# Performance work log

Measured on AMD Instinct MI355X. Metric: run time of the kernel, lower is better.

Reference implementation:

```python
import jax, jax.numpy as jnp
import numpy as np

LEAKY_ALPHA = 0.2  # tf.nn.leaky_relu default

B, N, F_IN, HID = 1, 8192, 512, 256


def setup_inputs() -> dict:
    key = jax.random.key(0)
    ks = jax.random.split(key, 4)
    seq = jax.random.normal(ks[0], (B, N, F_IN), dtype=jnp.float32)
    bias_mat = jnp.zeros((B, N, N), dtype=jnp.float32)  # 0 = edge present (fully connected mask)
    W = jax.random.normal(ks[1], (F_IN, HID), dtype=jnp.float32) * (1.0 / np.sqrt(F_IN))
    a1 = jax.random.normal(ks[2], (HID, 1), dtype=jnp.float32) * (1.0 / np.sqrt(HID))
    b1 = jnp.zeros((1,), dtype=jnp.float32)
    a2 = jax.random.normal(ks[3], (HID, 1), dtype=jnp.float32) * (1.0 / np.sqrt(HID))
    b2 = jnp.zeros((1,), dtype=jnp.float32)
    bias_zero = jnp.zeros((HID,), dtype=jnp.float32)
    return {"seq": seq, "bias_mat": bias_mat, "W": W, "a1": a1, "b1": b1,
            "a2": a2, "b2": b2, "bias_zero": bias_zero}


def reference(seq, bias_mat, W, a1, b1, a2, b2, bias_zero):
    # Conv1D(kernel=1, no bias) == per-node linear projection
    seq_fts = jnp.einsum('bnf,fh->bnh', seq, W)            # [B,N,H]
    f_1 = jnp.einsum('bnh,ho->bno', seq_fts, a1) + b1      # [B,N,1]
    f_2 = jnp.einsum('bnh,ho->bno', seq_fts, a2) + b2      # [B,N,1]
    logits = f_1 + jnp.swapaxes(f_2, 1, 2)                 # [B,N,N] outer-sum
    scores = jnp.where(logits > 0, logits, LEAKY_ALPHA * logits) + bias_mat
    coefs = jax.nn.softmax(scores, axis=-1)                # masked softmax over neighbors
    vals = jnp.einsum('bnm,bmh->bnh', coefs, seq_fts)      # aggregation
    ret = vals + bias_zero
    return jax.nn.elu(ret)
```

## Files before the change

### kernel.cpp

```cpp
#include <hip/hip_runtime.h>
#include <hip/hip_bf16.h>
#include <stdint.h>

#define NN 8192
#define FIN 512
#define HID 256

typedef short bf16x8 __attribute__((ext_vector_type(8)));
typedef float f32x4 __attribute__((ext_vector_type(4)));

__device__ __forceinline__ uint32_t pk2(float lo, float hi) {
  uint32_t a = __float_as_uint(lo), b = __float_as_uint(hi);
  a = (a + 0x7FFFu + ((a >> 16) & 1u)) >> 16;
  b = (b + 0x7FFFu + ((b >> 16) & 1u)) >> 16;
  return a | (b << 16);
}

#define OFF_SEQB   0u
#define OFF_WTB    8388608u
#define OFF_FTST   8650752u
#define OFF_F1     12845056u
#define OFF_F2     12877824u
#define OFF_Z      12910592u
#define OFF_F2MAX  12943360u

__global__ void k_cvt_seq(const float* __restrict__ seq, short* __restrict__ seqb) {
  int i = (blockIdx.x * 256 + threadIdx.x) * 4;
  float4 v = *(const float4*)(seq + i);
  uint2 o; o.x = pk2(v.x, v.y); o.y = pk2(v.z, v.w);
  *(uint2*)(seqb + i) = o;
}

__global__ void k_wt(const float* __restrict__ W, short* __restrict__ WTb) {
  int h = blockIdx.x;
  int t = threadIdx.x;
  int k = t * 2;
  float w0 = W[k * 256 + h], w1 = W[(k + 1) * 256 + h];
  ((uint32_t*)(WTb + h * 512))[t] = pk2(w0, w1);
}

__global__ __launch_bounds__(256) void k_proj(
    const short* __restrict__ seqb, const short* __restrict__ WTb,
    const float* __restrict__ a1, const float* __restrict__ b1,
    const float* __restrict__ a2, const float* __restrict__ b2,
    short* __restrict__ ftsP, float* __restrict__ f1g, float* __restrict__ f2g,
    uint32_t* __restrict__ f2maxenc) {
  __shared__ short At[64][72];
  __shared__ float f1a[64], f2a[64];
  const int t = threadIdx.x;
  const int l = t & 63, w = t >> 6;
  const int lr = l & 15, lg = l >> 4;
  const int R0 = blockIdx.x * 64;
  const int srow = t >> 2, scol = (t & 3) * 16;
  f32x4 acc[4][4] = {};
  if (t < 64) { f1a[t] = 0.f; f2a[t] = 0.f; }
  for (int kt = 0; kt < FIN; kt += 64) {
    uint4 s0 = *(const uint4*)(seqb + (size_t)(R0 + srow) * FIN + kt + scol);
    uint4 s1 = *(const uint4*)(seqb + (size_t)(R0 + srow) * FIN + kt + scol + 8);
    __syncthreads();
    *(uint4*)&At[srow][scol] = s0;
    *(uint4*)&At[srow][scol + 8] = s1;
    __syncthreads();
#pragma unroll
    for (int kk = 0; kk < 2; ++kk) {
      bf16x8 af[4];
#pragma unroll
      for (int mf = 0; mf < 4; ++mf)
        af[mf] = *(const bf16x8*)&At[mf * 16 + lr][kk * 32 + lg * 8];
#pragma unroll
      for (int nf = 0; nf < 4; ++nf) {
        int h = w * 64 + nf * 16 + lr;
        bf16x8 bfr = *(const bf16x8*)(WTb + h * FIN + kt + kk * 32 + lg * 8);
#pragma unroll
        for (int mf = 0; mf < 4; ++mf)
          acc[mf][nf] = __builtin_amdgcn_mfma_f32_16x16x32_bf16(af[mf], bfr, acc[mf][nf], 0, 0, 0);
      }
    }
  }
  __syncthreads();
  float a1v[4], a2v[4];
#pragma unroll
  for (int nf = 0; nf < 4; ++nf) {
    int h = w * 64 + nf * 16 + lr;
    a1v[nf] = a1[h]; a2v[nf] = a2[h];
  }
#pragma unroll
  for (int mf = 0; mf < 4; ++mf) {
    const int jo = mf * 16 + lg * 4;
    const int slot = (jo >> 3) ^ (lr & 7);
#pragma unroll
    for (int nf = 0; nf < 4; ++nf) {
      int h = w * 64 + nf * 16 + lr;
      uint2 o; o.x = pk2(acc[mf][nf][0], acc[mf][nf][1]);
      o.y = pk2(acc[mf][nf][2], acc[mf][nf][3]);
      *(uint2*)(ftsP + (size_t)blockIdx.x * 16384 + h * 64 + slot * 8 + (jo & 7)) = o;
    }
#pragma unroll
    for (int e = 0; e < 4; ++e) {
      float p1 = 0.f, p2 = 0.f;
#pragma unroll
      for (int nf = 0; nf < 4; ++nf) { p1 += acc[mf][nf][e] * a1v[nf]; p2 += acc[mf][nf][e] * a2v[nf]; }
#pragma unroll
      for (int m = 8; m >= 1; m >>= 1) { p1 += __shfl_xor(p1, m, 16); p2 += __shfl_xor(p2, m, 16); }
      if (lr == 0) {
        atomicAdd(&f1a[mf * 16 + lg * 4 + e], p1);
        atomicAdd(&f2a[mf * 16 + lg * 4 + e], p2);
      }
    }
  }
  __syncthreads();
  if (t < 64) {
    float v1 = f1a[t] + b1[0];
    float v2 = f2a[t] + b2[0];
    f1g[R0 + t] = v1; f2g[R0 + t] = v2;
    uint32_t u = __float_as_uint(v2);
    u = (u & 0x80000000u) ? ~u : (u | 0x80000000u);
    atomicMax(f2maxenc, u);
  }
}

__global__ __launch_bounds__(256, 2) void k_flash(
    const float* __restrict__ bias, const short* __restrict__ ftsP,
    const float* __restrict__ f1g, const float* __restrict__ f2g,
    const uint32_t* __restrict__ f2maxenc,
    float* __restrict__ outacc, float* __restrict__ Zg) {
  __shared__ short Vb[2][16384];
  const int t = threadIdx.x;
  const int l = t & 63, wid = t >> 6;
  const int lr = l & 15, lg = l >> 4;
  const int rbase = blockIdx.x * 128 + wid * 32;
  const int rowA = rbase + lr;
  const int jbase = blockIdx.y * 1024;
  const int jt0 = jbase >> 6;
  const int NT = 16;

  uint32_t ue = *f2maxenc;
  float f2mx = __uint_as_float((ue & 0x80000000u) ? (ue ^ 0x80000000u) : ~ue);
  float f1v0 = f1g[rowA];
  float f1v1 = f1g[rowA + 16];
  float x0 = f1v0 + f2mx, x1 = f1v1 + f2mx;
  float mr0 = fmaxf(x0, 0.2f * x0);
  float mr1 = fmaxf(x1, 0.2f * x1);

  const float* bp0 = bias + (size_t)rowA * NN + jbase + lg * 8;
  const float* bp1 = bp0 + (size_t)16 * NN;
  const float* qp = f2g + jbase + lg * 8;

  const int s0 = lg ^ (lr & 7);
  const int s1 = s0 ^ 4;

  f32x4 acc0[16] = {};
  f32x4 acc1[16] = {};
  float z0 = 0.f, z1 = 0.f;
  float4 bb0[2][2], bb1[2][2], qq[2][2];

#define STAGE(TT, BUF)                                                          \
  if ((TT) < NT) {                                                              \
    const short* gs = ftsP + (size_t)(jt0 + (TT)) * 16384 + wid * 4096 + l * 8; \
    _Pragma("unroll")                                                           \
    for (int c = 0; c < 8; ++c)                                                 \
      __builtin_amdgcn_global_load_lds(                                         \
          (const __attribute__((address_space(1))) void*)(gs + c * 512),        \
          (__attribute__((address_space(3))) void*)&Vb[(BUF)][wid * 4096 + c * 512], \
          16, 0, 0);                                                            \
  }
#define LOADB(TT)                                                               \
  if ((TT) < NT) {                                                              \
    _Pragma("unroll")                                                           \
    for (int kk = 0; kk < 2; ++kk) {                                            \
      _Pragma("unroll")                                                         \
      for (int h = 0; h < 2; ++h) {                                             \
        bb0[kk][h] = *(const float4*)(bp0 + (TT) * 64 + kk * 32 + h * 4);       \
        bb1[kk][h] = *(const float4*)(bp1 + (TT) * 64 + kk * 32 + h * 4);       \
        qq[kk][h]  = *(const float4*)(qp  + (TT) * 64 + kk * 32 + h * 4);       \
      }                                                                         \
    }                                                                           \
  }
#define EHALF(F1V, MR, BBK, QQK, ZACC, AOUT)                                    \
  {                                                                             \
    float p[8];                                                                 \
    _Pragma("unroll")                                                           \
    for (int e = 0; e < 4; ++e) {                                               \
      float s = (F1V) + ((const float*)&QQK[0])[e];                             \
      float ls = fmaxf(s, 0.2f * s);                                            \
      p[e] = __expf(ls + ((const float*)&BBK[0])[e] - (MR));                    \
    }                                                                           \
    _Pragma("unroll")                                                           \
    for (int e = 0; e < 4; ++e) {                                               \
      float s = (F1V) + ((const float*)&QQK[1])[e];                             \
      float ls = fmaxf(s, 0.2f * s);                                            \
      p[4 + e] = __expf(ls + ((const float*)&BBK[1])[e] - (MR));                \
    }                                                                           \
    ZACC += ((p[0] + p[1]) + (p[2] + p[3])) + ((p[4] + p[5]) + (p[6] + p[7]));  \
    union { bf16x8 v; uint32_t u[4]; } A;                                       \
    A.u[0] = pk2(p[0], p[1]); A.u[1] = pk2(p[2], p[3]);                         \
    A.u[2] = pk2(p[4], p[5]); A.u[3] = pk2(p[6], p[7]);                         \
    AOUT = A.v;                                                                 \
  }

  STAGE(0, 0)
  STAGE(1, 1)
  LOADB(0)
  __syncthreads();

  for (int tt = 0; tt < NT; ++tt) {
    bf16x8 A0k0, A0k1, A1k0, A1k1;
    EHALF(f1v0, mr0, bb0[0], qq[0], z0, A0k0)
    EHALF(f1v0, mr0, bb0[1], qq[1], z0, A0k1)
    EHALF(f1v1, mr1, bb1[0], qq[0], z1, A1k0)
    EHALF(f1v1, mr1, bb1[1], qq[1], z1, A1k1)

    LOADB(tt + 1)

    {
      const int cb = tt & 1;
      const short* vr0 = &Vb[cb][lr * 64 + s0 * 8];
      const short* vr1 = &Vb[cb][lr * 64 + s1 * 8];
#pragma unroll
      for (int nf = 0; nf < 16; ++nf) {
        bf16x8 B0 = *(const bf16x8*)(vr0 + nf * 1024);
        acc0[nf] = __builtin_amdgcn_mfma_f32_16x16x32_bf16(A0k0, B0, acc0[nf], 0, 0, 0);
        acc1[nf] = __builtin_amdgcn_mfma_f32_16x16x32_bf16(A1k0, B0, acc1[nf], 0, 0, 0);
      }
#pragma unroll
      for (int nf = 0; nf < 16; ++nf) {
        bf16x8 B1 = *(const bf16x8*)(vr1 + nf * 1024);
        acc0[nf] = __builtin_amdgcn_mfma_f32_16x16x32_bf16(A0k1, B1, acc0[nf], 0, 0, 0);
        acc1[nf] = __builtin_amdgcn_mfma_f32_16x16x32_bf16(A1k1, B1, acc1[nf], 0, 0, 0);
      }
    }

    __syncthreads();
    STAGE(tt + 2, tt & 1)
  }
#undef STAGE
#undef LOADB
#undef EHALF

  z0 += __shfl_xor(z0, 16); z0 += __shfl_xor(z0, 32);
  z1 += __shfl_xor(z1, 16); z1 += __shfl_xor(z1, 32);
  if (lg == 0) {
    atomicAdd(&Zg[rowA], z0);
    atomicAdd(&Zg[rowA + 16], z1);
  }

#pragma unroll
  for (int nf = 0; nf < 16; ++nf) {
    int col = nf * 16 + lr;
#pragma unroll
    for (int e = 0; e < 4; ++e) {
      atomicAdd(&outacc[(size_t)(rbase + lg * 4 + e) * HID + col], acc0[nf][e]);
      atomicAdd(&outacc[(size_t)(rbase + 16 + lg * 4 + e) * HID + col], acc1[nf][e]);
    }
  }
}

__global__ void k_final(float* __restrict__ outp, const float* __restrict__ Zg,
                        const float* __restrict__ bz) {
  int i4 = (blockIdx.x * 256 + threadIdx.x) * 4;
  int row = i4 >> 8;
  int col = i4 & 255;
  float4 v = *(float4*)(outp + i4);
  float zr = 1.0f / Zg[row];
  float4 b = *(const float4*)(bz + col);
  float r[4] = {v.x * zr + b.x, v.y * zr + b.y, v.z * zr + b.z, v.w * zr + b.w};
#pragma unroll
  for (int e = 0; e < 4; ++e) r[e] = r[e] > 0.f ? r[e] : (__expf(r[e]) - 1.f);
  *(float4*)(outp + i4) = make_float4(r[0], r[1], r[2], r[3]);
}

extern "C" void kernel_launch(void* const* d_in, const int* in_sizes, int n_in,
                              void* d_out, int out_size, void* d_ws, size_t ws_size,
                              hipStream_t stream) {
  const float* seq  = (const float*)d_in[0];
  const float* bias = (const float*)d_in[1];
  const float* W    = (const float*)d_in[2];
  const float* a1   = (const float*)d_in[3];
  const float* b1   = (const float*)d_in[4];
  const float* a2   = (const float*)d_in[5];
  const float* b2   = (const float*)d_in[6];
  const float* bz   = (const float*)d_in[7];
  float* out = (float*)d_out;
  char* ws = (char*)d_ws;
  short* seqb = (short*)(ws + OFF_SEQB);
  short* WTb  = (short*)(ws + OFF_WTB);
  short* ftsP = (short*)(ws + OFF_FTST);
  float* f1g  = (float*)(ws + OFF_F1);
  float* f2g  = (float*)(ws + OFF_F2);
  float* Zg   = (float*)(ws + OFF_Z);
  uint32_t* f2m = (uint32_t*)(ws + OFF_F2MAX);

  hipMemsetAsync(d_out, 0, (size_t)NN * HID * 4, stream);
  hipMemsetAsync(Zg, 0, NN * 4, stream);
  hipMemsetAsync(f2m, 0, 4, stream);

  k_cvt_seq<<<4096, 256, 0, stream>>>(seq, seqb);
  k_wt<<<256, 256, 0, stream>>>(W, WTb);
  k_proj<<<128, 256, 0, stream>>>(seqb, WTb, a1, b1, a2, b2, ftsP, f1g, f2g, f2m);
  k_flash<<<dim3(64, 8), 256, 0, stream>>>(bias, ftsP, f1g, f2g, f2m, out, Zg);
  k_final<<<2048, 256, 0, stream>>>(out, Zg, bz);
}
```

Baseline: 174.1 us.

## Repartition flash kernel: 8 waves split output columns, fewer rows per wave

The attention kernel now runs 512-thread blocks of 64 rows over 2048 key columns, instead of 256-thread blocks of 128 rows over 1024 columns. Each wave owns 16 rows and half of the 256 output columns, so per-wave accumulator registers are cut by four and occupancy can rise. The cost is that the exp/score work for each row is computed twice (once per column half), bias is read twice per row, and the block has more waves sharing each barrier. Fewer column splits also halves the atomic traffic into the output.

Measured after the change: 186.0 us. 1.07x slower.

```diff
diff --git a/kernel.cpp b/kernel.cpp
--- a/kernel.cpp
+++ b/kernel.cpp
@@ -119,7 +119,7 @@
   }
 }
 
-__global__ __launch_bounds__(256, 2) void k_flash(
+__global__ __launch_bounds__(512, 4) void k_flash(
     const float* __restrict__ bias, const short* __restrict__ ftsP,
     const float* __restrict__ f1g, const float* __restrict__ f2g,
     const uint32_t* __restrict__ f2maxenc,
@@ -128,40 +128,39 @@
   const int t = threadIdx.x;
   const int l = t & 63, wid = t >> 6;
   const int lr = l & 15, lg = l >> 4;
-  const int rbase = blockIdx.x * 128 + wid * 32;
+  const int hh = wid & 1;
+  const int rg = wid >> 1;
+  const int rbase = blockIdx.x * 64 + rg * 16;
   const int rowA = rbase + lr;
-  const int jbase = blockIdx.y * 1024;
+  const int jbase = blockIdx.y * 2048;
   const int jt0 = jbase >> 6;
-  const int NT = 16;
+  const int NT = 32;
+  const int nfb = hh * 8;
 
   uint32_t ue = *f2maxenc;
   float f2mx = __uint_as_float((ue & 0x80000000u) ? (ue ^ 0x80000000u) : ~ue);
-  float f1v0 = f1g[rowA];
-  float f1v1 = f1g[rowA + 16];
-  float x0 = f1v0 + f2mx, x1 = f1v1 + f2mx;
-  float mr0 = fmaxf(x0, 0.2f * x0);
-  float mr1 = fmaxf(x1, 0.2f * x1);
-
-  const float* bp0 = bias + (size_t)rowA * NN + jbase + lg * 8;
-  const float* bp1 = bp0 + (size_t)16 * NN;
+  float f1v = f1g[rowA];
+  float xm = f1v + f2mx;
+  float mr = fmaxf(xm, 0.2f * xm);
+
+  const float* bp = bias + (size_t)rowA * NN + jbase + lg * 8;
   const float* qp = f2g + jbase + lg * 8;
 
   const int s0 = lg ^ (lr & 7);
   const int s1 = s0 ^ 4;
 
-  f32x4 acc0[16] = {};
-  f32x4 acc1[16] = {};
-  float z0 = 0.f, z1 = 0.f;
-  float4 bb0[2][2], bb1[2][2], qq[2][2];
+  f32x4 acc[8] = {};
+  float z = 0.f;
+  float4 bb[2][2], qq[2][2];
 
 #define STAGE(TT, BUF)                                                          \
   if ((TT) < NT) {                                                              \
-    const short* gs = ftsP + (size_t)(jt0 + (TT)) * 16384 + wid * 4096 + l * 8; \
-    _Pragma("unroll")                                                           \
-    for (int c = 0; c < 8; ++c)                                                 \
+    const short* gs = ftsP + (size_t)(jt0 + (TT)) * 16384 + wid * 2048 + l * 8; \
+    _Pragma("unroll")                                                           \
+    for (int c = 0; c < 4; ++c)                                                 \
       __builtin_amdgcn_global_load_lds(                                         \
           (const __attribute__((address_space(1))) void*)(gs + c * 512),        \
-          (__attribute__((address_space(3))) void*)&Vb[(BUF)][wid * 4096 + c * 512], \
+          (__attribute__((address_space(3))) void*)&Vb[(BUF)][wid * 2048 + c * 512], \
           16, 0, 0);                                                            \
   }
 #define LOADB(TT)                                                               \
@@ -169,29 +168,28 @@
     _Pragma("unroll")                                                           \
     for (int kk = 0; kk < 2; ++kk) {                                            \
       _Pragma("unroll")                                                         \
-      for (int h = 0; h < 2; ++h) {                                             \
-        bb0[kk][h] = *(const float4*)(bp0 + (TT) * 64 + kk * 32 + h * 4);       \
-        bb1[kk][h] = *(const float4*)(bp1 + (TT) * 64 + kk * 32 + h * 4);       \
-        qq[kk][h]  = *(const float4*)(qp  + (TT) * 64 + kk * 32 + h * 4);       \
+      for (int h4 = 0; h4 < 2; ++h4) {                                          \
+        bb[kk][h4] = *(const float4*)(bp + (TT) * 64 + kk * 32 + h4 * 4);       \
+        qq[kk][h4] = *(const float4*)(qp + (TT) * 64 + kk * 32 + h4 * 4);       \
       }                                                                         \
     }                                                                           \
   }
-#define EHALF(F1V, MR, BBK, QQK, ZACC, AOUT)                                    \
+#define EHALF(BBK, QQK, AOUT)                                                   \
   {                                                                             \
     float p[8];                                                                 \
     _Pragma("unroll")                                                           \
     for (int e = 0; e < 4; ++e) {                                               \
-      float s = (F1V) + ((const float*)&QQK[0])[e];                             \
+      float s = f1v + ((const float*)&QQK[0])[e];                               \
       float ls = fmaxf(s, 0.2f * s);                                            \
-      p[e] = __expf(ls + ((const float*)&BBK[0])[e] - (MR));                    \
+      p[e] = __expf(ls + ((const float*)&BBK[0])[e] - mr);                      \
     }                                                                           \
     _Pragma("unroll")                                                           \
     for (int e = 0; e < 4; ++e) {                                               \
-      float s = (F1V) + ((const float*)&QQK[1])[e];                             \
+      float s = f1v + ((const float*)&QQK[1])[e];                               \
       float ls = fmaxf(s, 0.2f * s);                                            \
-      p[4 + e] = __expf(ls + ((const float*)&BBK[1])[e] - (MR));                \
+      p[4 + e] = __expf(ls + ((const float*)&BBK[1])[e] - mr);                  \
     }                                                                           \
-    ZACC += ((p[0] + p[1]) + (p[2] + p[3])) + ((p[4] + p[5]) + (p[6] + p[7]));  \
+    z += ((p[0] + p[1]) + (p[2] + p[3])) + ((p[4] + p[5]) + (p[6] + p[7]));     \
     union { bf16x8 v; uint32_t u[4]; } A;                                       \
     A.u[0] = pk2(p[0], p[1]); A.u[1] = pk2(p[2], p[3]);                         \
     A.u[2] = pk2(p[4], p[5]); A.u[3] = pk2(p[6], p[7]);                         \
@@ -204,11 +202,9 @@
   __syncthreads();
 
   for (int tt = 0; tt < NT; ++tt) {
-    bf16x8 A0k0, A0k1, A1k0, A1k1;
-    EHALF(f1v0, mr0, bb0[0], qq[0], z0, A0k0)
-    EHALF(f1v0, mr0, bb0[1], qq[1], z0, A0k1)
-    EHALF(f1v1, mr1, bb1[0], qq[0], z1, A1k0)
-    EHALF(f1v1, mr1, bb1[1], qq[1], z1, A1k1)
+    bf16x8 A0, A1;
+    EHALF(bb[0], qq[0], A0)
+    EHALF(bb[1], qq[1], A1)
 
     LOADB(tt + 1)
 
@@ -217,16 +213,14 @@
       const short* vr0 = &Vb[cb][lr * 64 + s0 * 8];
       const short* vr1 = &Vb[cb][lr * 64 + s1 * 8];
 #pragma unroll
-      for (int nf = 0; nf < 16; ++nf) {
-        bf16x8 B0 = *(const bf16x8*)(vr0 + nf * 1024);
-        acc0[nf] = __builtin_amdgcn_mfma_f32_16x16x32_bf16(A0k0, B0, acc0[nf], 0, 0, 0);
-        acc1[nf] = __builtin_amdgcn_mfma_f32_16x16x32_bf16(A1k0, B0, acc1[nf], 0, 0, 0);
-      }
-#pragma unroll
-      for (int nf = 0; nf < 16; ++nf) {
-        bf16x8 B1 = *(const bf16x8*)(vr1 + nf * 1024);
-        acc0[nf] = __builtin_amdgcn_mfma_f32_16x16x32_bf16(A0k1, B1, acc0[nf], 0, 0, 0);
-        acc1[nf] = __builtin_amdgcn_mfma_f32_16x16x32_bf16(A1k1, B1, acc1[nf], 0, 0, 0);
+      for (int nf = 0; nf < 8; ++nf) {
+        bf16x8 B0 = *(const bf16x8*)(vr0 + (nfb + nf) * 1024);
+        acc[nf] = __builtin_amdgcn_mfma_f32_16x16x32_bf16(A0, B0, acc[nf], 0, 0, 0);
+      }
+#pragma unroll
+      for (int nf = 0; nf < 8; ++nf) {
+        bf16x8 B1 = *(const bf16x8*)(vr1 + (nfb + nf) * 1024);
+        acc[nf] = __builtin_amdgcn_mfma_f32_16x16x32_bf16(A1, B1, acc[nf], 0, 0, 0);
       }
     }
 
@@ -237,21 +231,16 @@
 #undef LOADB
 #undef EHALF
 
-  z0 += __shfl_xor(z0, 16); z0 += __shfl_xor(z0, 32);
-  z1 += __shfl_xor(z1, 16); z1 += __shfl_xor(z1, 32);
-  if (lg == 0) {
-    atomicAdd(&Zg[rowA], z0);
-    atomicAdd(&Zg[rowA + 16], z1);
-  }
-
-#pragma unroll
-  for (int nf = 0; nf < 16; ++nf) {
-    int col = nf * 16 + lr;
-#pragma unroll
-    for (int e = 0; e < 4; ++e) {
-      atomicAdd(&outacc[(size_t)(rbase + lg * 4 + e) * HID + col], acc0[nf][e]);
-      atomicAdd(&outacc[(size_t)(rbase + 16 + lg * 4 + e) * HID + col], acc1[nf][e]);
-    }
+  z += __shfl_xor(z, 16);
+  z += __shfl_xor(z, 32);
+  if (hh == 0 && lg == 0) atomicAdd(&Zg[rowA], z);
+
+#pragma unroll
+  for (int nf = 0; nf < 8; ++nf) {
+    int col = (nfb + nf) * 16 + lr;
+#pragma unroll
+    for (int e = 0; e < 4; ++e)
+      atomicAdd(&outacc[(size_t)(rbase + lg * 4 + e) * HID + col], acc[nf][e]);
   }
 }
 
@@ -297,6 +286,6 @@
   k_cvt_seq<<<4096, 256, 0, stream>>>(seq, seqb);
   k_wt<<<256, 256, 0, stream>>>(W, WTb);
   k_proj<<<128, 256, 0, stream>>>(seqb, WTb, a1, b1, a2, b2, ftsP, f1g, f2g, f2m);
-  k_flash<<<dim3(64, 8), 256, 0, stream>>>(bias, ftsP, f1g, f2g, f2m, out, Zg);
+  k_flash<<<dim3(128, 4), 512, 0, stream>>>(bias, ftsP, f1g, f2g, f2m, out, Zg);
   k_final<<<2048, 256, 0, stream>>>(out, Zg, bz);
 }
```

## Split flash kernel output columns across wave pairs and deepen prefetch pipeline

Applied to the files above, without the earlier changes.

The flash-attention kernel now assigns two waves to each 32-row group, each handling half of the 256 output columns, so each block covers 64 rows over a 2048-column key range. This halves the accumulator registers per wave and the number of output atomics per key range. The loop is unrolled by two with double-buffered bias/f2 register prefetch two tiles ahead, a partial vmcnt wait instead of a full syncthreads, and setprio around the MFMA section. In exchange, each wave recomputes exponentials for its rows (the softmax work is duplicated across the two waves of a pair) and the bias matrix is read twice.

After: 484.6 us. 2.78x slower.

```diff
diff --git a/kernel.cpp b/kernel.cpp
--- a/kernel.cpp
+++ b/kernel.cpp
@@ -128,11 +128,14 @@
   const int t = threadIdx.x;
   const int l = t & 63, wid = t >> 6;
   const int lr = l & 15, lg = l >> 4;
-  const int rbase = blockIdx.x * 128 + wid * 32;
+  const int hh = wid & 1;
+  const int rg = wid >> 1;
+  const int rbase = blockIdx.x * 64 + rg * 32;
   const int rowA = rbase + lr;
-  const int jbase = blockIdx.y * 1024;
+  const int jbase = blockIdx.y * 2048;
   const int jt0 = jbase >> 6;
-  const int NT = 16;
+  const int NT = 32;
+  const int nfb = hh * 8;
 
   uint32_t ue = *f2maxenc;
   float f2mx = __uint_as_float((ue & 0x80000000u) ? (ue ^ 0x80000000u) : ~ue);
@@ -149,10 +152,11 @@
   const int s0 = lg ^ (lr & 7);
   const int s1 = s0 ^ 4;
 
-  f32x4 acc0[16] = {};
-  f32x4 acc1[16] = {};
+  f32x4 acc0[8] = {};
+  f32x4 acc1[8] = {};
   float z0 = 0.f, z1 = 0.f;
-  float4 bb0[2][2], bb1[2][2], qq[2][2];
+  float4 bbA[2][2][2], qqA[2][2];
+  float4 bbB[2][2][2], qqB[2][2];
 
 #define STAGE(TT, BUF)                                                          \
   if ((TT) < NT) {                                                              \
@@ -164,32 +168,32 @@
           (__attribute__((address_space(3))) void*)&Vb[(BUF)][wid * 4096 + c * 512], \
           16, 0, 0);                                                            \
   }
-#define LOADB(TT)                                                               \
+#define LOADB(TT, BB, QQ)                                                       \
   if ((TT) < NT) {                                                              \
     _Pragma("unroll")                                                           \
     for (int kk = 0; kk < 2; ++kk) {                                            \
       _Pragma("unroll")                                                         \
-      for (int h = 0; h < 2; ++h) {                                             \
-        bb0[kk][h] = *(const float4*)(bp0 + (TT) * 64 + kk * 32 + h * 4);       \
-        bb1[kk][h] = *(const float4*)(bp1 + (TT) * 64 + kk * 32 + h * 4);       \
-        qq[kk][h]  = *(const float4*)(qp  + (TT) * 64 + kk * 32 + h * 4);       \
+      for (int h4 = 0; h4 < 2; ++h4) {                                          \
+        BB[0][kk][h4] = *(const float4*)(bp0 + (TT) * 64 + kk * 32 + h4 * 4);   \
+        BB[1][kk][h4] = *(const float4*)(bp1 + (TT) * 64 + kk * 32 + h4 * 4);   \
+        QQ[kk][h4]    = *(const float4*)(qp  + (TT) * 64 + kk * 32 + h4 * 4);   \
       }                                                                         \
     }                                                                           \
   }
-#define EHALF(F1V, MR, BBK, QQK, ZACC, AOUT)                                    \
+#define EHALF(F1V, MR, B0, B1, Q0, Q1, ZACC, AOUT)                              \
   {                                                                             \
     float p[8];                                                                 \
     _Pragma("unroll")                                                           \
     for (int e = 0; e < 4; ++e) {                                               \
-      float s = (F1V) + ((const float*)&QQK[0])[e];                             \
+      float s = (F1V) + ((const float*)&(Q0))[e];                               \
       float ls = fmaxf(s, 0.2f * s);                                            \
-      p[e] = __expf(ls + ((const float*)&BBK[0])[e] - (MR));                    \
+      p[e] = __expf(ls + ((const float*)&(B0))[e] - (MR));                      \
     }                                                                           \
     _Pragma("unroll")                                                           \
     for (int e = 0; e < 4; ++e) {                                               \
-      float s = (F1V) + ((const float*)&QQK[1])[e];                             \
+      float s = (F1V) + ((const float*)&(Q1))[e];                               \
       float ls = fmaxf(s, 0.2f * s);                                            \
-      p[4 + e] = __expf(ls + ((const float*)&BBK[1])[e] - (MR));                \
+      p[4 + e] = __expf(ls + ((const float*)&(B1))[e] - (MR));                  \
     }                                                                           \
     ZACC += ((p[0] + p[1]) + (p[2] + p[3])) + ((p[4] + p[5]) + (p[6] + p[7]));  \
     union { bf16x8 v; uint32_t u[4]; } A;                                       \
@@ -197,56 +201,65 @@
     A.u[2] = pk2(p[4], p[5]); A.u[3] = pk2(p[6], p[7]);                         \
     AOUT = A.v;                                                                 \
   }
+#define ITER(TT, BB, QQ, CUR)                                                   \
+  {                                                                             \
+    bf16x8 A00, A01, A10, A11;                                                  \
+    EHALF(f1v0, mr0, BB[0][0][0], BB[0][0][1], QQ[0][0], QQ[0][1], z0, A00)     \
+    EHALF(f1v0, mr0, BB[0][1][0], BB[0][1][1], QQ[1][0], QQ[1][1], z0, A01)     \
+    EHALF(f1v1, mr1, BB[1][0][0], BB[1][0][1], QQ[0][0], QQ[0][1], z1, A10)     \
+    EHALF(f1v1, mr1, BB[1][1][0], BB[1][1][1], QQ[1][0], QQ[1][1], z1, A11)     \
+    LOADB((TT) + 2, BB, QQ)                                                     \
+    __builtin_amdgcn_s_setprio(1);                                              \
+    {                                                                           \
+      const short* vr0 = &Vb[(CUR)][lr * 64 + s0 * 8];                          \
+      const short* vr1 = &Vb[(CUR)][lr * 64 + s1 * 8];                          \
+      _Pragma("unroll")                                                         \
+      for (int nf = 0; nf < 8; ++nf) {                                          \
+        bf16x8 B0 = *(const bf16x8*)(vr0 + (nfb + nf) * 1024);                  \
+        acc0[nf] = __builtin_amdgcn_mfma_f32_16x16x32_bf16(A00, B0, acc0[nf], 0, 0, 0); \
+        acc1[nf] = __builtin_amdgcn_mfma_f32_16x16x32_bf16(A10, B0, acc1[nf], 0, 0, 0); \
+      }                                                                         \
+      _Pragma("unroll")                                                         \
+      for (int nf = 0; nf < 8; ++nf) {                                          \
+        bf16x8 B1 = *(const bf16x8*)(vr1 + (nfb + nf) * 1024);                  \
+        acc0[nf] = __builtin_amdgcn_mfma_f32_16x16x32_bf16(A01, B1, acc0[nf], 0, 0, 0); \
+        acc1[nf] = __builtin_amdgcn_mfma_f32_16x16x32_bf16(A11, B1, acc1[nf], 0, 0, 0); \
+      }                                                                         \
+    }                                                                           \
+    __builtin_amdgcn_s_setprio(0);                                              \
+    __builtin_amdgcn_sched_barrier(0);                                          \
+    asm volatile("s_waitcnt vmcnt(12)");                                        \
+    __builtin_amdgcn_sched_barrier(0);                                          \
+    __builtin_amdgcn_s_barrier();                                               \
+    __builtin_amdgcn_sched_barrier(0);                                          \
+    STAGE((TT) + 2, (CUR))                                                      \
+  }
 
   STAGE(0, 0)
+  LOADB(0, bbA, qqA)
   STAGE(1, 1)
-  LOADB(0)
+  LOADB(1, bbB, qqB)
   __syncthreads();
 
-  for (int tt = 0; tt < NT; ++tt) {
-    bf16x8 A0k0, A0k1, A1k0, A1k1;
-    EHALF(f1v0, mr0, bb0[0], qq[0], z0, A0k0)
-    EHALF(f1v0, mr0, bb0[1], qq[1], z0, A0k1)
-    EHALF(f1v1, mr1, bb1[0], qq[0], z1, A1k0)
-    EHALF(f1v1, mr1, bb1[1], qq[1], z1, A1k1)
-
-    LOADB(tt + 1)
-
-    {
-      const int cb = tt & 1;
-      const short* vr0 = &Vb[cb][lr * 64 + s0 * 8];
-      const short* vr1 = &Vb[cb][lr * 64 + s1 * 8];
-#pragma unroll
-      for (int nf = 0; nf < 16; ++nf) {
-        bf16x8 B0 = *(const bf16x8*)(vr0 + nf * 1024);
-        acc0[nf] = __builtin_amdgcn_mfma_f32_16x16x32_bf16(A0k0, B0, acc0[nf], 0, 0, 0);
-        acc1[nf] = __builtin_amdgcn_mfma_f32_16x16x32_bf16(A1k0, B0, acc1[nf], 0, 0, 0);
-      }
-#pragma unroll
-      for (int nf = 0; nf < 16; ++nf) {
-        bf16x8 B1 = *(const bf16x8*)(vr1 + nf * 1024);
-        acc0[nf] = __builtin_amdgcn_mfma_f32_16x16x32_bf16(A0k1, B1, acc0[nf], 0, 0, 0);
-        acc1[nf] = __builtin_amdgcn_mfma_f32_16x16x32_bf16(A1k1, B1, acc1[nf], 0, 0, 0);
-      }
-    }
-
-    __syncthreads();
-    STAGE(tt + 2, tt & 1)
-  }
+  for (int tt = 0; tt < NT; tt += 2) {
+    ITER(tt, bbA, qqA, 0)
+    ITER(tt + 1, bbB, qqB, 1)
+  }
+#undef ITER
+#undef EHALF
+#undef LOADB
 #undef STAGE
-#undef LOADB
-#undef EHALF
 
   z0 += __shfl_xor(z0, 16); z0 += __shfl_xor(z0, 32);
   z1 += __shfl_xor(z1, 16); z1 += __shfl_xor(z1, 32);
-  if (lg == 0) {
+  if (hh == 0 && lg == 0) {
     atomicAdd(&Zg[rowA], z0);
     atomicAdd(&Zg[rowA + 16], z1);
   }
 
 #pragma unroll
-  for (int nf = 0; nf < 16; ++nf) {
-    int col = nf * 16 + lr;
+  for (int nf = 0; nf < 8; ++nf) {
+    int col = (nfb + nf) * 16 + lr;
 #pragma unroll
     for (int e = 0; e < 4; ++e) {
       atomicAdd(&outacc[(size_t)(rbase + lg * 4 + e) * HID + col], acc0[nf][e]);
@@ -297,6 +310,6 @@
   k_cvt_seq<<<4096, 256, 0, stream>>>(seq, seqb);
   k_wt<<<256, 256, 0, stream>>>(W, WTb);
   k_proj<<<128, 256, 0, stream>>>(seqb, WTb, a1, b1, a2, b2, ftsP, f1g, f2g, f2m);
-  k_flash<<<dim3(64, 8), 256, 0, stream>>>(bias, ftsP, f1g, f2g, f2m, out, Zg);
+  k_flash<<<dim3(128, 4), 256, 0, stream>>>(bias, ftsP, f1g, f2g, f2m, out, Zg);
   k_final<<<2048, 256, 0, stream>>>(out, Zg, bz);
 }
```
